# Kernel optimization log

Hardware: AMD Instinct MI355X
Metric: run time of the kernel (lower is better)

## Reference

```python
import jax, jax.numpy as jnp
import numpy as np

ENDING = False  # ending=False -> 'outgoing' triangle update; True -> 'incoming'
EPS = 1e-5


def _ln(x, w, b):
    m = jnp.mean(x, axis=-1, keepdims=True)
    v = jnp.mean((x - m) ** 2, axis=-1, keepdims=True)
    return (x - m) * jax.lax.rsqrt(v + EPS) * w + b


def setup_inputs() -> dict:
    key = jax.random.key(0)
    ks = jax.random.split(key, 6)
    B, N, D = 1, 384, 128
    s = 0.02
    return {
        "x": jax.random.normal(ks[0], (B, N, N, D), jnp.float32),
        "norm_in_w": jnp.ones((D,), jnp.float32),
        "norm_in_b": jnp.zeros((D,), jnp.float32),
        "w_g_in": jax.random.normal(ks[1], (2 * D, D), jnp.float32) * s,
        "w_p_in": jax.random.normal(ks[2], (2 * D, D), jnp.float32) * s,
        "w_g_out": jax.random.normal(ks[3], (D, D), jnp.float32) * s,
        "norm_out_w": jnp.ones((D,), jnp.float32),
        "norm_out_b": jnp.zeros((D,), jnp.float32),
        "w_p_out": jax.random.normal(ks[4], (D, D), jnp.float32) * s,
    }


def reference(x, norm_in_w, norm_in_b, w_g_in, w_p_in, w_g_out,
              norm_out_w, norm_out_b, w_p_out):
    D = x.shape[-1]
    xn = _ln(x, norm_in_w, norm_in_b)                       # [B,N,N,D]
    g_in = jax.nn.sigmoid(jnp.einsum('bijd,ed->bije', xn, w_g_in))  # [B,N,N,2D]
    p = jnp.einsum('bijd,ed->bije', xn, w_p_in) * g_in      # [B,N,N,2D]
    a, b = p[..., :D], p[..., D:]
    if ENDING:
        # incoming: out[i,j,d] = sum_k a[k,i,d] * b[k,j,d]
        t = jnp.einsum('bkid,bkjd->bijd', a, b)
    else:
        # outgoing: out[i,j,d] = sum_k a[i,k,d] * b[j,k,d]
        t = jnp.einsum('bikd,bjkd->bijd', a, b)
    g_out = jax.nn.sigmoid(jnp.einsum('bijd,ed->bije', xn, w_g_out))  # [B,N,N,D]
    return g_out * jnp.einsum('bijd,ed->bije', _ln(t, norm_out_w, norm_out_b), w_p_out)
```

## Files before the change

### kernel.cpp

```cpp
#include <hip/hip_runtime.h>
#include <hip/hip_bf16.h>
#include <math.h>

#define NPOS 147456
#define NSEQ 384

typedef __attribute__((ext_vector_type(4))) float f32x4;
typedef __attribute__((ext_vector_type(8))) short bf16x8;
typedef __attribute__((ext_vector_type(4))) short s16x4;

__device__ __forceinline__ unsigned short f2bf(float f){
  union { float f; unsigned u; } v; v.f = f;
  unsigned r = v.u + 0x7FFFu + ((v.u >> 16) & 1u);
  return (unsigned short)(r >> 16);
}
__device__ __forceinline__ float bf2f(unsigned short h){
  union { unsigned u; float f; } v; v.u = ((unsigned)h) << 16;
  return v.f;
}
__device__ __forceinline__ float fastsig(float x){
  return __builtin_amdgcn_rcpf(1.0f + __expf(-x));
}
__device__ __forceinline__ unsigned pk2(float lo, float hi){
  return (unsigned)f2bf(lo) | ((unsigned)f2bf(hi) << 16);
}

__global__ void wswz_all(const float* __restrict__ wgi, const float* __restrict__ wpi,
                         const float* __restrict__ wgo, const float* __restrict__ wpo,
                         unsigned short* __restrict__ wgi_s, unsigned short* __restrict__ wpi_s,
                         unsigned short* __restrict__ wgo_s, unsigned short* __restrict__ wpo_s){
  int i = blockIdx.x * 256 + threadIdx.x;
  int t = i >> 11;
  int r = i & 2047;
  const float* src; unsigned short* dst; int lt;
  if (t < 16)      { src = wgi; dst = wgi_s; lt = t;      }
  else if (t < 32) { src = wpi; dst = wpi_s; lt = t - 16; }
  else if (t < 40) { src = wgo; dst = wgo_s; lt = t - 32; }
  else             { src = wpo; dst = wpo_s; lt = t - 40; }
  int j = r & 7, lane = (r >> 3) & 63, kk = (r >> 9) & 3;
  int lrow = lane & 15, khh = lane >> 4;
  dst[lt*2048 + r] = f2bf(src[(lt*16 + lrow)*128 + kk*32 + khh*8 + j]);
}

__global__ __launch_bounds__(256, 3) void k1_ln_proj(
    const float* __restrict__ x,
    const float* __restrict__ ln_w, const float* __restrict__ ln_b,
    const unsigned short* __restrict__ wg_sw,
    const unsigned short* __restrict__ wp_sw,
    const unsigned short* __restrict__ wgo_sw,
    unsigned short* __restrict__ a_t,
    unsigned short* __restrict__ b_t,
    unsigned short* __restrict__ g_t)
{
  __shared__ unsigned short xn[128][128];
  unsigned short (*obuf)[16][136] = reinterpret_cast<unsigned short(*)[16][136]>(&xn[0][0]);

  const int tid  = threadIdx.x;
  const int posb = blockIdx.x * 128;
  const int lane = tid & 63;
  const int wid  = tid >> 6;

  const int rql = tid >> 2;
  const int q   = tid & 3;
  #pragma unroll
  for (int rr = 0; rr < 2; ++rr){
    int row = rr*64 + rql;
    const float* xr = x + (size_t)(posb + row) * 128 + q * 32;
    float v[32]; float s = 0.f, s2 = 0.f;
    #pragma unroll
    for (int j2 = 0; j2 < 8; ++j2){
      f32x4 t4 = *(const f32x4*)(xr + j2*4);
      #pragma unroll
      for (int m = 0; m < 4; ++m){ float f = t4[m]; v[j2*4+m] = f; s += f; s2 += f*f; }
    }
    s  += __shfl_xor(s, 1);  s  += __shfl_xor(s, 2);
    s2 += __shfl_xor(s2, 1); s2 += __shfl_xor(s2, 2);
    float mean = s * (1.f/128.f);
    float rstd = rsqrtf(s2 * (1.f/128.f) - mean*mean + 1e-5f);
    int sw = (row & 7) * 8;
    #pragma unroll
    for (int c = 0; c < 4; ++c){
      float n[8];
      #pragma unroll
      for (int j2 = 0; j2 < 8; ++j2){
        int k = q*32 + c*8 + j2;
        n[j2] = (v[c*8+j2] - mean) * rstd * ln_w[k] + ln_b[k];
      }
      uint4 u;
      u.x = pk2(n[0], n[1]); u.y = pk2(n[2], n[3]);
      u.z = pk2(n[4], n[5]); u.w = pk2(n[6], n[7]);
      *(uint4*)&xn[row][(q*32 + c*8) ^ sw] = u;
    }
  }
  __syncthreads();

  const int lrow = lane & 15, kh = lane >> 4;
  bf16x8 afrag[2][4];
  #pragma unroll
  for (int r = 0; r < 2; ++r){
    int row = wid*32 + r*16 + lrow;
    int sw = (row & 7) * 8;
    #pragma unroll
    for (int kk = 0; kk < 4; ++kk)
      afrag[r][kk] = *(const bf16x8*)&xn[row][(kk*32 + kh*8) ^ sw];
  }
  __syncthreads();

  const int kh4 = kh * 4;
  const int scl = wid*4 + kh;
  const int spo = lrow * 8;

#define LOADW_PAIR(G, P, et) do { \
    const unsigned short* _wg = wg_sw + (size_t)(et)*2048 + lane*8; \
    const unsigned short* _wp = wp_sw + (size_t)(et)*2048 + lane*8; \
    _Pragma("unroll") \
    for (int kk = 0; kk < 4; ++kk){ \
      G[kk] = *(const bf16x8*)(_wg + kk*512); \
      P[kk] = *(const bf16x8*)(_wp + kk*512); \
    } } while(0)

#define COMPUTE_PAIR(G, P, et) do { \
    f32x4 accg0 = {0.f,0.f,0.f,0.f}, accg1 = {0.f,0.f,0.f,0.f}; \
    f32x4 accp0 = {0.f,0.f,0.f,0.f}, accp1 = {0.f,0.f,0.f,0.f}; \
    _Pragma("unroll") \
    for (int kk = 0; kk < 4; ++kk){ \
      accg0 = __builtin_amdgcn_mfma_f32_16x16x32_bf16(afrag[0][kk], G[kk], accg0, 0, 0, 0); \
      accg1 = __builtin_amdgcn_mfma_f32_16x16x32_bf16(afrag[1][kk], G[kk], accg1, 0, 0, 0); \
      accp0 = __builtin_amdgcn_mfma_f32_16x16x32_bf16(afrag[0][kk], P[kk], accp0, 0, 0, 0); \
      accp1 = __builtin_amdgcn_mfma_f32_16x16x32_bf16(afrag[1][kk], P[kk], accp1, 0, 0, 0); \
    } \
    { uint2 u0, u1; \
      u0.x = pk2(fastsig(accg0[0])*accp0[0], fastsig(accg0[1])*accp0[1]); \
      u0.y = pk2(fastsig(accg0[2])*accp0[2], fastsig(accg0[3])*accp0[3]); \
      u1.x = pk2(fastsig(accg1[0])*accp1[0], fastsig(accg1[1])*accp1[1]); \
      u1.y = pk2(fastsig(accg1[2])*accp1[2], fastsig(accg1[3])*accp1[3]); \
      *(uint2*)&obuf[(et)&1][lrow][wid*32 + kh4]      = u0; \
      *(uint2*)&obuf[(et)&1][lrow][wid*32 + 16 + kh4] = u1; } \
    __syncthreads(); \
    { bf16x8 vv = *(const bf16x8*)&obuf[(et)&1][scl][spo]; \
      int colg = (et)*16 + scl; \
      unsigned short* dst = ((et) < 8) ? (a_t + (size_t)colg * NPOS) \
                                       : (b_t + (size_t)(colg - 128) * NPOS); \
      *(bf16x8*)(dst + posb + spo) = vv; } \
  } while(0)

  {
    bf16x8 gA[4], pA[4], gB[4], pB[4];
    LOADW_PAIR(gA, pA, 0);
    #pragma unroll
    for (int e2 = 0; e2 < 8; ++e2){
      LOADW_PAIR(gB, pB, e2*2 + 1);
      COMPUTE_PAIR(gA, pA, e2*2);
      if (e2 < 7) LOADW_PAIR(gA, pA, e2*2 + 2);
      COMPUTE_PAIR(gB, pB, e2*2 + 1);
    }
  }

#define LOADW_G(Q, et) do { \
    const unsigned short* _wq = wgo_sw + (size_t)(et)*2048 + lane*8; \
    _Pragma("unroll") \
    for (int kk = 0; kk < 4; ++kk) Q[kk] = *(const bf16x8*)(_wq + kk*512); \
  } while(0)

#define COMPUTE_G(Q, et) do { \
    f32x4 a0 = {0.f,0.f,0.f,0.f}, a1 = {0.f,0.f,0.f,0.f}; \
    _Pragma("unroll") \
    for (int kk = 0; kk < 4; ++kk){ \
      a0 = __builtin_amdgcn_mfma_f32_16x16x32_bf16(afrag[0][kk], Q[kk], a0, 0, 0, 0); \
      a1 = __builtin_amdgcn_mfma_f32_16x16x32_bf16(afrag[1][kk], Q[kk], a1, 0, 0, 0); \
    } \
    { uint2 u0, u1; \
      u0.x = pk2(fastsig(a0[0]), fastsig(a0[1])); \
      u0.y = pk2(fastsig(a0[2]), fastsig(a0[3])); \
      u1.x = pk2(fastsig(a1[0]), fastsig(a1[1])); \
      u1.y = pk2(fastsig(a1[2]), fastsig(a1[3])); \
      *(uint2*)&obuf[(et)&1][lrow][wid*32 + kh4]      = u0; \
      *(uint2*)&obuf[(et)&1][lrow][wid*32 + 16 + kh4] = u1; } \
    __syncthreads(); \
    { bf16x8 vv = *(const bf16x8*)&obuf[(et)&1][scl][spo]; \
      *(bf16x8*)(g_t + (size_t)((et)*16 + scl) * NPOS + posb + spo) = vv; } \
  } while(0)

  {
    bf16x8 qA[4], qB[4];
    LOADW_G(qA, 0);
    #pragma unroll
    for (int e2 = 0; e2 < 4; ++e2){
      LOADW_G(qB, e2*2 + 1);
      COMPUTE_G(qA, e2*2);
      if (e2 < 3) LOADW_G(qA, e2*2 + 2);
      COMPUTE_G(qB, e2*2 + 1);
    }
  }
#undef LOADW_PAIR
#undef COMPUTE_PAIR
#undef LOADW_G
#undef COMPUTE_G
}

#define K2PAD 56
__global__ __launch_bounds__(256) void k2_tri(
    const unsigned short* __restrict__ a_t,
    const unsigned short* __restrict__ b_t,
    unsigned short* __restrict__ t_t)
{
  __shared__ unsigned short As[128][K2PAD];
  __shared__ unsigned short Bs[128][K2PAD];

  const int d  = blockIdx.z;
  const int i0 = blockIdx.y * 128;
  const int j0 = blockIdx.x * 128;
  const unsigned short* Ab = a_t + (size_t)d * NPOS;
  const unsigned short* Bb = b_t + (size_t)d * NPOS;

  const int tid = threadIdx.x;
  const int wid = tid >> 6, lane = tid & 63;
  const int wr = wid >> 1, wc = wid & 1;
  const int lrow = lane & 15, kh = (lane >> 4) * 8;

  f32x4 acc[4][4];
  #pragma unroll
  for (int r = 0; r < 4; ++r)
    #pragma unroll
    for (int c = 0; c < 4; ++c)
      acc[r][c] = (f32x4){0.f,0.f,0.f,0.f};

  const int sr = tid >> 1, sc = (tid & 1) * 16;

  for (int k0 = 0; k0 < NSEQ; k0 += 32){
    bf16x8 va0 = *(const bf16x8*)(Ab + (size_t)(i0 + sr) * NSEQ + k0 + sc);
    bf16x8 va1 = *(const bf16x8*)(Ab + (size_t)(i0 + sr) * NSEQ + k0 + sc + 8);
    bf16x8 vb0 = *(const bf16x8*)(Bb + (size_t)(j0 + sr) * NSEQ + k0 + sc);
    bf16x8 vb1 = *(const bf16x8*)(Bb + (size_t)(j0 + sr) * NSEQ + k0 + sc + 8);
    __syncthreads();
    *(bf16x8*)&As[sr][sc]     = va0;
    *(bf16x8*)&As[sr][sc + 8] = va1;
    *(bf16x8*)&Bs[sr][sc]     = vb0;
    *(bf16x8*)&Bs[sr][sc + 8] = vb1;
    __syncthreads();

    bf16x8 af[4], bfr[4];
    #pragma unroll
    for (int r = 0; r < 4; ++r)
      af[r] = *(const bf16x8*)&As[wr*64 + r*16 + lrow][kh];
    #pragma unroll
    for (int c = 0; c < 4; ++c)
      bfr[c] = *(const bf16x8*)&Bs[wc*64 + c*16 + lrow][kh];
    #pragma unroll
    for (int r = 0; r < 4; ++r)
      #pragma unroll
      for (int c = 0; c < 4; ++c)
        acc[r][c] = __builtin_amdgcn_mfma_f32_16x16x32_bf16(af[r], bfr[c], acc[r][c], 0, 0, 0);
  }

  unsigned short* Tb = t_t + (size_t)d * NPOS;
  #pragma unroll
  for (int r = 0; r < 4; ++r){
    int i = i0 + wr*64 + r*16 + (lane >> 4) * 4;
    #pragma unroll
    for (int c = 0; c < 4; ++c){
      int j = j0 + wc*64 + c*16 + lrow;
      #pragma unroll
      for (int jj = 0; jj < 4; ++jj)
        Tb[(size_t)(i + jj) * NSEQ + j] = f2bf(acc[r][c][jj]);
    }
  }
}

#define LNS 136
__global__ __launch_bounds__(256, 3) void k3_out(
    const unsigned short* __restrict__ t_t,
    const unsigned short* __restrict__ g_t,
    const float* __restrict__ ln_w, const float* __restrict__ ln_b,
    const unsigned short* __restrict__ wpo_sw,
    float* __restrict__ out)
{
  __shared__ unsigned short traw[128][136];
  __shared__ float regB[9024];
  __shared__ float smean[128], srs[128];

  const int tid = threadIdx.x;
  const int p0  = blockIdx.x * 128;
  const int lane = tid & 63, wid = tid >> 6;

  float* pps = regB;
  float* ppq = regB + 2048;
  unsigned short* lnt = (unsigned short*)regB;
  float (*ltile)[68] = (float(*)[68])regB;

  {
    int d = tid >> 1, c0 = (tid & 1) * 64;
    const unsigned short* src = t_t + (size_t)d * NPOS + p0 + c0;
    #pragma unroll
    for (int j = 0; j < 8; ++j)
      *(bf16x8*)&traw[d][c0 + j*8] = *(const bf16x8*)(src + j*8);
  }
  __syncthreads();

  const int pg = tid & 15, dh = tid >> 4;
  {
    float s8[8] = {0,0,0,0,0,0,0,0}, q8[8] = {0,0,0,0,0,0,0,0};
    #pragma unroll
    for (int jd = 0; jd < 8; ++jd){
      bf16x8 v = *(const bf16x8*)&traw[dh*8 + jd][pg*8];
      #pragma unroll
      for (int p = 0; p < 8; ++p){
        float f = bf2f((unsigned short)v[p]);
        s8[p] += f; q8[p] += f*f;
      }
    }
    #pragma unroll
    for (int p = 0; p < 8; ++p){
      pps[dh*128 + pg*8 + p] = s8[p];
      ppq[dh*128 + pg*8 + p] = q8[p];
    }
  }
  __syncthreads();
  if (tid < 128){
    float s = 0.f, q = 0.f;
    #pragma unroll
    for (int k = 0; k < 16; ++k){ s += pps[k*128 + tid]; q += ppq[k*128 + tid]; }
    float m = s * (1.f/128.f);
    smean[tid] = m;
    srs[tid]   = rsqrtf(q * (1.f/128.f) - m*m + 1e-5f);
  }
  __syncthreads();

  {
    float vv[8][8];
    #pragma unroll
    for (int jd = 0; jd < 8; ++jd){
      bf16x8 v = *(const bf16x8*)&traw[dh*8 + jd][pg*8];
      float w = ln_w[dh*8 + jd], bb = ln_b[dh*8 + jd];
      #pragma unroll
      for (int p = 0; p < 8; ++p)
        vv[jd][p] = (bf2f((unsigned short)v[p]) - smean[pg*8+p]) * srs[pg*8+p] * w + bb;
    }
    #pragma unroll
    for (int p = 0; p < 8; ++p){
      uint4 u;
      u.x = pk2(vv[0][p], vv[1][p]); u.y = pk2(vv[2][p], vv[3][p]);
      u.z = pk2(vv[4][p], vv[5][p]); u.w = pk2(vv[6][p], vv[7][p]);
      *(uint4*)&lnt[(size_t)(pg*8 + p)*LNS + dh*8] = u;
    }
  }
  __syncthreads();

  const int lrow = lane & 15, kh = (lane >> 4) * 8;
  bf16x8 af[2][4];
  #pragma unroll
  for (int r = 0; r < 2; ++r)
    #pragma unroll
    for (int kk = 0; kk < 4; ++kk)
      af[r][kk] = *(const bf16x8*)&lnt[(size_t)(wid*32 + r*16 + lrow)*LNS + kk*32 + kh];
  __syncthreads();

  {
    int e = tid >> 1, c0 = (tid & 1) * 64;
    const unsigned short* src = g_t + (size_t)e * NPOS + p0 + c0;
    #pragma unroll
    for (int j = 0; j < 8; ++j)
      *(bf16x8*)&traw[e][c0 + j*8] = *(const bf16x8*)(src + j*8);
  }
  __syncthreads();

  #pragma unroll
  for (int half = 0; half < 2; ++half){
    #pragma unroll
    for (int cf4 = 0; cf4 < 4; ++cf4){
      int cf = half*4 + cf4;
      const unsigned short* wq = wpo_sw + (size_t)cf*2048 + lane*8;
      bf16x8 bfr[4];
      #pragma unroll
      for (int kk = 0; kk < 4; ++kk)
        bfr[kk] = *(const bf16x8*)(wq + kk*512);
      f32x4 a0 = {0.f,0.f,0.f,0.f}, a1 = {0.f,0.f,0.f,0.f};
      #pragma unroll
      for (int kk = 0; kk < 4; ++kk){
        a0 = __builtin_amdgcn_mfma_f32_16x16x32_bf16(af[0][kk], bfr[kk], a0, 0, 0, 0);
        a1 = __builtin_amdgcn_mfma_f32_16x16x32_bf16(af[1][kk], bfr[kk], a1, 0, 0, 0);
      }
      int e = cf*16 + lrow;
      #pragma unroll
      for (int r = 0; r < 2; ++r){
        f32x4 av = r ? a1 : a0;
        int prow = wid*32 + r*16 + (lane >> 4)*4;
        #pragma unroll
        for (int jj = 0; jj < 4; ++jj){
          float g = bf2f(traw[e][prow + jj]);
          ltile[prow + jj][cf4*16 + lrow] = g * av[jj];
        }
      }
    }
    __syncthreads();
    {
      int pos = tid >> 1, he = tid & 1;
      const float* srcp = &ltile[pos][he*32];
      float* dst = out + (size_t)(p0 + pos)*128 + half*64 + he*32;
      #pragma unroll
      for (int j = 0; j < 8; ++j)
        *(f32x4*)(dst + j*4) = *(const f32x4*)(srcp + j*4);
    }
    __syncthreads();
  }
}

extern "C" void kernel_launch(void* const* d_in, const int* in_sizes, int n_in,
                              void* d_out, int out_size, void* d_ws, size_t ws_size,
                              hipStream_t stream) {
  (void)in_sizes; (void)n_in; (void)out_size; (void)ws_size;
  const float* x   = (const float*)d_in[0];
  const float* niw = (const float*)d_in[1];
  const float* nib = (const float*)d_in[2];
  const float* wgi = (const float*)d_in[3];
  const float* wpi = (const float*)d_in[4];
  const float* wgo = (const float*)d_in[5];
  const float* now = (const float*)d_in[6];
  const float* nob = (const float*)d_in[7];
  const float* wpo = (const float*)d_in[8];
  float* out = (float*)d_out;

  unsigned short* a_t   = (unsigned short*)d_ws;
  unsigned short* b_t   = a_t + (size_t)128 * NPOS;
  unsigned short* g_t   = b_t + (size_t)128 * NPOS;
  unsigned short* t_t   = g_t + (size_t)128 * NPOS;
  unsigned short* wgi_s = t_t + (size_t)128 * NPOS;
  unsigned short* wpi_s = wgi_s + 256 * 128;
  unsigned short* wgo_s = wpi_s + 256 * 128;
  unsigned short* wpo_s = wgo_s + 128 * 128;

  wswz_all<<<384, 256, 0, stream>>>(wgi, wpi, wgo, wpo, wgi_s, wpi_s, wgo_s, wpo_s);

  k1_ln_proj<<<NPOS/128, 256, 0, stream>>>(x, niw, nib, wgi_s, wpi_s, wgo_s, a_t, b_t, g_t);

  dim3 g2(3, 3, 128);
  k2_tri<<<g2, 256, 0, stream>>>(a_t, b_t, t_t);

  k3_out<<<NPOS/128, 256, 0, stream>>>(t_t, g_t, now, nob, wpo_s, out);
}
```

Measured before the change: 168.2 us.

## Stage k1 projection weights through LDS via async global_load_lds double buffering

The LN+projection kernel now stages each 16-column weight tile into shared memory with direct global-to-LDS loads and double buffering, instead of each wave loading the tiles into registers. The loops are no longer manually unrolled. This cuts register pressure, so the occupancy hint rises from 3 to 4 blocks per CU. The tradeoff is extra LDS reads per MFMA step and a reliance on the barrier ordering to make the async LDS writes visible. A missing vmcnt wait before the barrier could make this racy.

```diff
diff --git a/kernel.cpp b/kernel.cpp
--- a/kernel.cpp
+++ b/kernel.cpp
@@ -23,6 +23,11 @@
 }
 __device__ __forceinline__ unsigned pk2(float lo, float hi){
   return (unsigned)f2bf(lo) | ((unsigned)f2bf(hi) << 16);
+}
+__device__ __forceinline__ void gl16(const unsigned short* g, unsigned short* l){
+  __builtin_amdgcn_global_load_lds(
+      (const __attribute__((address_space(1))) void*)g,
+      (__attribute__((address_space(3))) void*)l, 16, 0, 0);
 }
 
 __global__ void wswz_all(const float* __restrict__ wgi, const float* __restrict__ wpi,
@@ -42,7 +47,7 @@
   dst[lt*2048 + r] = f2bf(src[(lt*16 + lrow)*128 + kk*32 + khh*8 + j]);
 }
 
-__global__ __launch_bounds__(256, 3) void k1_ln_proj(
+__global__ __launch_bounds__(256, 4) void k1_ln_proj(
     const float* __restrict__ x,
     const float* __restrict__ ln_w, const float* __restrict__ ln_b,
     const unsigned short* __restrict__ wg_sw,
@@ -53,7 +58,8 @@
     unsigned short* __restrict__ g_t)
 {
   __shared__ unsigned short xn[128][128];
-  unsigned short (*obuf)[16][136] = reinterpret_cast<unsigned short(*)[16][136]>(&xn[0][0]);
+  unsigned short* wbuf = &xn[0][0];
+  unsigned short* obuf = wbuf + 8192;
 
   const int tid  = threadIdx.x;
   const int posb = blockIdx.x * 128;
@@ -109,93 +115,83 @@
   const int kh4 = kh * 4;
   const int scl = wid*4 + kh;
   const int spo = lrow * 8;
-
-#define LOADW_PAIR(G, P, et) do { \
-    const unsigned short* _wg = wg_sw + (size_t)(et)*2048 + lane*8; \
-    const unsigned short* _wp = wp_sw + (size_t)(et)*2048 + lane*8; \
-    _Pragma("unroll") \
-    for (int kk = 0; kk < 4; ++kk){ \
-      G[kk] = *(const bf16x8*)(_wg + kk*512); \
-      P[kk] = *(const bf16x8*)(_wp + kk*512); \
-    } } while(0)
-
-#define COMPUTE_PAIR(G, P, et) do { \
-    f32x4 accg0 = {0.f,0.f,0.f,0.f}, accg1 = {0.f,0.f,0.f,0.f}; \
-    f32x4 accp0 = {0.f,0.f,0.f,0.f}, accp1 = {0.f,0.f,0.f,0.f}; \
-    _Pragma("unroll") \
-    for (int kk = 0; kk < 4; ++kk){ \
-      accg0 = __builtin_amdgcn_mfma_f32_16x16x32_bf16(afrag[0][kk], G[kk], accg0, 0, 0, 0); \
-      accg1 = __builtin_amdgcn_mfma_f32_16x16x32_bf16(afrag[1][kk], G[kk], accg1, 0, 0, 0); \
-      accp0 = __builtin_amdgcn_mfma_f32_16x16x32_bf16(afrag[0][kk], P[kk], accp0, 0, 0, 0); \
-      accp1 = __builtin_amdgcn_mfma_f32_16x16x32_bf16(afrag[1][kk], P[kk], accp1, 0, 0, 0); \
-    } \
-    { uint2 u0, u1; \
-      u0.x = pk2(fastsig(accg0[0])*accp0[0], fastsig(accg0[1])*accp0[1]); \
-      u0.y = pk2(fastsig(accg0[2])*accp0[2], fastsig(accg0[3])*accp0[3]); \
-      u1.x = pk2(fastsig(accg1[0])*accp1[0], fastsig(accg1[1])*accp1[1]); \
-      u1.y = pk2(fastsig(accg1[2])*accp1[2], fastsig(accg1[3])*accp1[3]); \
-      *(uint2*)&obuf[(et)&1][lrow][wid*32 + kh4]      = u0; \
-      *(uint2*)&obuf[(et)&1][lrow][wid*32 + 16 + kh4] = u1; } \
-    __syncthreads(); \
-    { bf16x8 vv = *(const bf16x8*)&obuf[(et)&1][scl][spo]; \
-      int colg = (et)*16 + scl; \
-      unsigned short* dst = ((et) < 8) ? (a_t + (size_t)colg * NPOS) \
-                                       : (b_t + (size_t)(colg - 128) * NPOS); \
-      *(bf16x8*)(dst + posb + spo) = vv; } \
+  const int wl8 = wid*512 + lane*8;
+
+#define STAGE_PAIR(et, b) do { \
+    gl16(wg_sw + (size_t)(et)*2048 + wl8, wbuf + (2*(b)+0)*2048 + wid*512); \
+    gl16(wp_sw + (size_t)(et)*2048 + wl8, wbuf + (2*(b)+1)*2048 + wid*512); \
   } while(0)
-
-  {
-    bf16x8 gA[4], pA[4], gB[4], pB[4];
-    LOADW_PAIR(gA, pA, 0);
-    #pragma unroll
-    for (int e2 = 0; e2 < 8; ++e2){
-      LOADW_PAIR(gB, pB, e2*2 + 1);
-      COMPUTE_PAIR(gA, pA, e2*2);
-      if (e2 < 7) LOADW_PAIR(gA, pA, e2*2 + 2);
-      COMPUTE_PAIR(gB, pB, e2*2 + 1);
-    }
-  }
-
-#define LOADW_G(Q, et) do { \
-    const unsigned short* _wq = wgo_sw + (size_t)(et)*2048 + lane*8; \
-    _Pragma("unroll") \
-    for (int kk = 0; kk < 4; ++kk) Q[kk] = *(const bf16x8*)(_wq + kk*512); \
+#define STAGE_G(et, b) do { \
+    gl16(wgo_sw + (size_t)(et)*2048 + wl8, wbuf + (b)*2048 + wid*512); \
   } while(0)
 
-#define COMPUTE_G(Q, et) do { \
-    f32x4 a0 = {0.f,0.f,0.f,0.f}, a1 = {0.f,0.f,0.f,0.f}; \
-    _Pragma("unroll") \
-    for (int kk = 0; kk < 4; ++kk){ \
-      a0 = __builtin_amdgcn_mfma_f32_16x16x32_bf16(afrag[0][kk], Q[kk], a0, 0, 0, 0); \
-      a1 = __builtin_amdgcn_mfma_f32_16x16x32_bf16(afrag[1][kk], Q[kk], a1, 0, 0, 0); \
-    } \
-    { uint2 u0, u1; \
-      u0.x = pk2(fastsig(a0[0]), fastsig(a0[1])); \
-      u0.y = pk2(fastsig(a0[2]), fastsig(a0[3])); \
-      u1.x = pk2(fastsig(a1[0]), fastsig(a1[1])); \
-      u1.y = pk2(fastsig(a1[2]), fastsig(a1[3])); \
-      *(uint2*)&obuf[(et)&1][lrow][wid*32 + kh4]      = u0; \
-      *(uint2*)&obuf[(et)&1][lrow][wid*32 + 16 + kh4] = u1; } \
-    __syncthreads(); \
-    { bf16x8 vv = *(const bf16x8*)&obuf[(et)&1][scl][spo]; \
-      *(bf16x8*)(g_t + (size_t)((et)*16 + scl) * NPOS + posb + spo) = vv; } \
-  } while(0)
-
-  {
-    bf16x8 qA[4], qB[4];
-    LOADW_G(qA, 0);
-    #pragma unroll
-    for (int e2 = 0; e2 < 4; ++e2){
-      LOADW_G(qB, e2*2 + 1);
-      COMPUTE_G(qA, e2*2);
-      if (e2 < 3) LOADW_G(qA, e2*2 + 2);
-      COMPUTE_G(qB, e2*2 + 1);
-    }
-  }
-#undef LOADW_PAIR
-#undef COMPUTE_PAIR
-#undef LOADW_G
-#undef COMPUTE_G
+  STAGE_PAIR(0, 0);
+  __syncthreads();
+
+  for (int et = 0; et < 16; ++et){
+    const int b = et & 1;
+    const unsigned short* wG = wbuf + (2*b+0)*2048 + lane*8;
+    const unsigned short* wP = wbuf + (2*b+1)*2048 + lane*8;
+    f32x4 accg0 = {0.f,0.f,0.f,0.f}, accg1 = {0.f,0.f,0.f,0.f};
+    f32x4 accp0 = {0.f,0.f,0.f,0.f}, accp1 = {0.f,0.f,0.f,0.f};
+    #pragma unroll
+    for (int kk = 0; kk < 4; ++kk){
+      bf16x8 G = *(const bf16x8*)(wG + kk*512);
+      bf16x8 P = *(const bf16x8*)(wP + kk*512);
+      accg0 = __builtin_amdgcn_mfma_f32_16x16x32_bf16(afrag[0][kk], G, accg0, 0, 0, 0);
+      accg1 = __builtin_amdgcn_mfma_f32_16x16x32_bf16(afrag[1][kk], G, accg1, 0, 0, 0);
+      accp0 = __builtin_amdgcn_mfma_f32_16x16x32_bf16(afrag[0][kk], P, accp0, 0, 0, 0);
+      accp1 = __builtin_amdgcn_mfma_f32_16x16x32_bf16(afrag[1][kk], P, accp1, 0, 0, 0);
+    }
+    {
+      uint2 u0, u1;
+      u0.x = pk2(fastsig(accg0[0])*accp0[0], fastsig(accg0[1])*accp0[1]);
+      u0.y = pk2(fastsig(accg0[2])*accp0[2], fastsig(accg0[3])*accp0[3]);
+      u1.x = pk2(fastsig(accg1[0])*accp1[0], fastsig(accg1[1])*accp1[1]);
+      u1.y = pk2(fastsig(accg1[2])*accp1[2], fastsig(accg1[3])*accp1[3]);
+      *(uint2*)&obuf[b*2176 + lrow*136 + wid*32 + kh4]      = u0;
+      *(uint2*)&obuf[b*2176 + lrow*136 + wid*32 + 16 + kh4] = u1;
+    }
+    if (et < 15) STAGE_PAIR(et+1, b^1);
+    else         STAGE_G(0, 0);
+    __syncthreads();
+    {
+      bf16x8 vv = *(const bf16x8*)&obuf[b*2176 + scl*136 + spo];
+      int colg = et*16 + scl;
+      unsigned short* dst = (et < 8) ? (a_t + (size_t)colg * NPOS)
+                                     : (b_t + (size_t)(colg - 128) * NPOS);
+      *(bf16x8*)(dst + posb + spo) = vv;
+    }
+  }
+
+  for (int gt = 0; gt < 8; ++gt){
+    const int b = gt & 1;
+    const unsigned short* wQ = wbuf + b*2048 + lane*8;
+    f32x4 a0 = {0.f,0.f,0.f,0.f}, a1 = {0.f,0.f,0.f,0.f};
+    #pragma unroll
+    for (int kk = 0; kk < 4; ++kk){
+      bf16x8 Q = *(const bf16x8*)(wQ + kk*512);
+      a0 = __builtin_amdgcn_mfma_f32_16x16x32_bf16(afrag[0][kk], Q, a0, 0, 0, 0);
+      a1 = __builtin_amdgcn_mfma_f32_16x16x32_bf16(afrag[1][kk], Q, a1, 0, 0, 0);
+    }
+    {
+      uint2 u0, u1;
+      u0.x = pk2(fastsig(a0[0]), fastsig(a0[1]));
+      u0.y = pk2(fastsig(a0[2]), fastsig(a0[3]));
+      u1.x = pk2(fastsig(a1[0]), fastsig(a1[1]));
+      u1.y = pk2(fastsig(a1[2]), fastsig(a1[3]));
+      *(uint2*)&obuf[b*2176 + lrow*136 + wid*32 + kh4]      = u0;
+      *(uint2*)&obuf[b*2176 + lrow*136 + wid*32 + 16 + kh4] = u1;
+    }
+    if (gt < 7) STAGE_G(gt+1, b^1);
+    __syncthreads();
+    {
+      bf16x8 vv = *(const bf16x8*)&obuf[b*2176 + scl*136 + spo];
+      *(bf16x8*)(g_t + (size_t)(gt*16 + scl) * NPOS + posb + spo) = vv;
+    }
+  }
+#undef STAGE_PAIR
+#undef STAGE_G
 }
 
 #define K2PAD 56
```

Measured after the change: 169.0 us. No clear change (+0.5%).
